# Kernel optimization log

Measured on AMD Instinct MI355X. Metric: run time of the kernel, lower is better.

## Reference

```python
import jax, jax.numpy as jnp
import numpy as np

KERNEL_BANDWIDTH = 0.3
STEP_SIZE = 0.5
NB_ITERATIONS = 4


def setup_inputs() -> dict:
    key = jax.random.key(0)
    # B x D x H x W pixel embeddings
    x_in = jax.random.normal(key, (2, 64, 96, 96), dtype=jnp.float32)
    return {"x_in": x_in}


def reference(x_in):
    B, D, H, W = x_in.shape
    N = H * W
    x0 = x_in.reshape(B, D, N)

    def body(x, _):
        # Gaussian-like kernel K[i,j] = exp(bw * <x_i, x_j>), symmetric NxN per batch
        K = jnp.exp(KERNEL_BANDWIDTH * jnp.einsum('bdn,bdm->bnm', x, x))  # (B,N,N)
        # torch: diag(K^T @ 1) then inverse of that diagonal == 1/column-sums
        colsum = jnp.sum(K, axis=1)  # (B,N)
        # x @ (K diag(1/colsum)): column-normalized weighted mean of embeddings
        xk = jnp.einsum('bdn,bnm->bdm', x, K) / colsum[:, None, :]
        x_new = STEP_SIZE * xk + (1.0 - STEP_SIZE) * x
        return x_new, x_new

    _, ys = jax.lax.scan(body, x0, None, length=NB_ITERATIONS)  # (I,B,D,N)
    allx = jnp.concatenate([x0[None], ys], axis=0)  # (I+1,B,D,N)
    # B x (I+1) x D x H x W
    return jnp.transpose(allx, (1, 0, 2, 3)).reshape(B, NB_ITERATIONS + 1, D, H, W)
```

## Files before the change

kernel.cpp:

```cpp
#include <hip/hip_runtime.h>
#include <hip/hip_bf16.h>

constexpr int B_    = 2;
constexpr int N_    = 9216;
constexpr int ITERS = 4;

constexpr int MTQ     = 128;
constexpr int MBF     = N_ / MTQ;
constexpr int KS      = 4;
constexpr int KEYS_WG = N_ / KS;
constexpr int KT      = 64;
constexpr int KTILES  = KEYS_WG / KT;
constexpr int NWG     = B_ * MBF * KS;
constexpr int PB      = 144;
constexpr int CGRID   = B_ * (N_ / 32);

constexpr float STEP = 0.5f;
constexpr float C2   = 0.43280851226668905f;

using short8   = __attribute__((ext_vector_type(8))) short;
using float16v = __attribute__((ext_vector_type(16))) float;
typedef __attribute__((ext_vector_type(2))) __bf16 bf16x2;

__device__ __forceinline__ unsigned short f2bf(float f) {
  union { float f; unsigned u; } v; v.f = f;
  unsigned u = v.u;
  unsigned r = (u + 0x7fffu + ((u >> 16) & 1u)) >> 16;
  return (unsigned short)r;
}

#if __has_builtin(__builtin_amdgcn_cvt_pk_bf16_f32)
__device__ __forceinline__ unsigned pk2bf(float a, float b) {
  bf16x2 r = __builtin_amdgcn_cvt_pk_bf16_f32(a, b);
  union { bf16x2 h; unsigned u; } v; v.h = r; return v.u;
}
#else
__device__ __forceinline__ unsigned pk2bf(float a, float b) {
  return (unsigned)f2bf(a) | ((unsigned)f2bf(b) << 16);
}
#endif

__device__ __forceinline__ float csum2(unsigned u, float cs) {
#if __has_builtin(__builtin_amdgcn_fdot2_f32_bf16)
  union { unsigned x; bf16x2 h; } a, o;
  a.x = u; o.x = 0x3f803f80u;
  return __builtin_amdgcn_fdot2_f32_bf16(a.h, o.h, cs, false);
#else
  union { unsigned u; float f; } lo, hi;
  lo.u = u << 16; hi.u = u & 0xffff0000u;
  return cs + lo.f + hi.f;
#endif
}

__device__ __forceinline__ void dma16(const unsigned short* g,
                                      unsigned short* lds_base, int lane) {
#if __has_builtin(__builtin_amdgcn_global_load_lds)
  __builtin_amdgcn_global_load_lds(
      (const __attribute__((address_space(1))) unsigned int*)g,
      (__attribute__((address_space(3))) unsigned int*)lds_base, 16, 0, 0);
#else
  *(int4*)((char*)lds_base + lane * 16) = *(const int4*)g;
#endif
}

__global__ void prep_kernel(const float* __restrict__ xin, float* __restrict__ out,
                            unsigned short* __restrict__ XT,
                            unsigned short* __restrict__ Xbf)
{
  const int bx = blockIdx.x;
  const int nb = bx % PB, b = bx / PB;
  const int n0 = nb * 64;
  const int tid = threadIdx.x;
  __shared__ float tile[64 * 65];

  #pragma unroll
  for (int r = 0; r < 16; ++r) {
    int idx = r * 256 + tid;
    int d = idx >> 6, j = idx & 63;
    float v = xin[((size_t)b * 64 + d) * N_ + n0 + j];
    out[(((size_t)b * 5 + 0) * 64 + d) * N_ + n0 + j] = v;
    Xbf[((size_t)b * 64 + d) * N_ + n0 + j] = f2bf(v);
    tile[d * 65 + j] = v;
  }
  __syncthreads();
  #pragma unroll
  for (int r = 0; r < 16; ++r) {
    int idx = r * 256 + tid;
    int nl = idx >> 6, d = idx & 63;
    XT[((size_t)b * N_ + n0 + nl) * 64 + d] = f2bf(tile[d * 65 + nl]);
  }
}

__global__ void __launch_bounds__(256, 3) flash_kernel(
    const unsigned short* __restrict__ XT,
    const unsigned short* __restrict__ Xbf,
    float* __restrict__ pacc, float* __restrict__ pcs)
{
  const int bx   = blockIdx.x;
  const int ks   = bx & 3;
  const int mb   = (bx >> 2) % MBF;
  const int b    = bx / (MBF * KS);
  const int tid  = threadIdx.x;
  const int wave = tid >> 6, lane = tid & 63;
  const int c = lane & 31, h = lane >> 5;
  const int cp = (c & 0x13) | ((c & 4) << 1) | ((c & 8) >> 1);
  const int m0 = mb * MTQ;
  const int bpaddr = (lane ^ 32) << 2;

  const unsigned short* XTb = XT  + (size_t)b * N_ * 64;
  const unsigned short* Xb  = Xbf + (size_t)b * 64 * N_;

  __shared__ __align__(16) unsigned short sXT[2][KT * 64];
  __shared__ __align__(16) unsigned short sXB[2][64 * KT];

  const int rr = lane >> 3, sc = lane & 7;
  const int gc = sc ^ rr;

  const int n0g0 = ks * KEYS_WG;

  const unsigned short* xtp  = XTb + (size_t)(n0g0 + wave * 16 + rr) * 64 + gc * 8;
  const unsigned short* xbp0 = Xb  + (size_t)(wave * 16 + rr) * N_ + n0g0 + gc * 8;
  const unsigned short* xbp1 = xbp0 + (size_t)8 * N_;

  auto stage = [&](int buf, const unsigned short* xt_,
                   const unsigned short* xb0_, const unsigned short* xb1_) {
    unsigned short* lt = &sXT[buf][wave * 16 * 64];
    unsigned short* lb = &sXB[buf][wave * 16 * 64];
    dma16(xt_,       lt,       lane);
    dma16(xt_ + 512, lt + 512, lane);
    dma16(xb0_,      lb,       lane);
    dma16(xb1_,      lb + 512, lane);
  };

  stage(0, xtp, xbp0, xbp1);
  xtp += KT * 64; xbp0 += KT; xbp1 += KT;

  short8 qf[4];
  #pragma unroll
  for (int k = 0; k < 4; ++k) {
    short8 raw = *(const short8*)(XTb +
        (size_t)(m0 + wave * 32 + c) * 64 + k * 16 + h * 8);
    unsigned o[4];
    const unsigned* rw = (const unsigned*)&raw;
    #pragma unroll
    for (int p4 = 0; p4 < 4; ++p4) {
      union { unsigned u; float f; } lo, hi;
      lo.u = rw[p4] << 16; hi.u = rw[p4] & 0xffff0000u;
      o[p4] = pk2bf(lo.f * C2, hi.f * C2);
    }
    qf[k] = *(const short8*)o;
  }

  const int e = cp & 7;
  const unsigned short* afb[4];
  #pragma unroll
  for (int k = 0; k < 4; ++k)
    afb[k] = &sXT[0][cp * 64 + ((2 * k + h) ^ e) * 8];
  const int ec = c & 7;
  const unsigned short* bfb0[2], * bfb1[2];
  #pragma unroll
  for (int s = 0; s < 2; ++s) {
    bfb0[s] = &sXB[0][c * 64 + ((4 * s +     h) ^ ec) * 8];
    bfb1[s] = &sXB[0][c * 64 + ((4 * s + 2 + h) ^ ec) * 8];
  }

  float16v zv;
  #pragma unroll
  for (int p = 0; p < 16; ++p) zv[p] = 0.f;
  float16v acc[2];
  acc[0] = zv; acc[1] = zv;
  float cs = 0.f;

  __syncthreads();

  #pragma unroll 2
  for (int t = 0; t < KTILES; ++t) {
    const int buf = t & 1;
    if (t + 1 < KTILES) {
      stage(buf ^ 1, xtp, xbp0, xbp1);
      xtp += KT * 64; xbp0 += KT; xbp1 += KT;
    }

    #pragma unroll
    for (int s = 0; s < 2; ++s) {
      short8 af[4];
      #pragma unroll
      for (int k = 0; k < 4; ++k)
        af[k] = *(const short8*)(afb[k] + buf * 4096 + s * 2048);

      float16v S = zv;
      #pragma unroll
      for (int k = 0; k < 4; ++k)
        S = __builtin_amdgcn_mfma_f32_32x32x16_bf16(af[k], qf[k], S, 0, 0, 0);

      unsigned q[8];
      #pragma unroll
      for (int g = 0; g < 8; ++g) {
        float w0 = __builtin_amdgcn_exp2f(S[2 * g]);
        float w1 = __builtin_amdgcn_exp2f(S[2 * g + 1]);
        unsigned u = pk2bf(w0, w1);
        q[g] = u;
        cs = csum2(u, cs);
      }

      union { unsigned d[4]; short8 s8; } a20, a21;
      a20.d[0] = q[0]; a20.d[1] = q[1]; a20.d[2] = q[2]; a20.d[3] = q[3];
      a21.d[0] = q[4]; a21.d[1] = q[5]; a21.d[2] = q[6]; a21.d[3] = q[7];

      short8 b20[2], b21[2];
      #pragma unroll
      for (int dt = 0; dt < 2; ++dt) {
        b20[dt] = *(const short8*)(bfb0[s] + buf * 4096 + dt * 2048);
        b21[dt] = *(const short8*)(bfb1[s] + buf * 4096 + dt * 2048);
      }
      #pragma unroll
      for (int dt = 0; dt < 2; ++dt)
        acc[dt] = __builtin_amdgcn_mfma_f32_32x32x16_bf16(a20.s8, b20[dt], acc[dt], 0, 0, 0);
      #pragma unroll
      for (int dt = 0; dt < 2; ++dt)
        acc[dt] = __builtin_amdgcn_mfma_f32_32x32x16_bf16(a21.s8, b21[dt], acc[dt], 0, 0, 0);
    }

    __syncthreads();
  }

  union { float f; int i; } cu; cu.f = cs;
  cu.i = __builtin_amdgcn_ds_bpermute(bpaddr, cu.i);
  float cst = cs + cu.f;
  if (h == 0) pcs[(size_t)bx * 128 + wave * 32 + c] = cst;

  float* pw = pacc + (size_t)bx * (MTQ * 64);
  #pragma unroll
  for (int dt = 0; dt < 2; ++dt)
    #pragma unroll
    for (int p = 0; p < 16; ++p) {
      int m = wave * 32 + (p & 3) + 8 * (p >> 2) + 4 * h;
      pw[m * 64 + dt * 32 + c] = acc[dt][p];
    }
}

__global__ void combine_kernel(const float* __restrict__ pacc,
                               const float* __restrict__ pcs,
                               float* __restrict__ out,
                               unsigned short* __restrict__ XT,
                               unsigned short* __restrict__ Xbf, int t)
{
  const int bx  = blockIdx.x;
  const int q32 = bx % 288, b = bx / 288;
  const int m0  = q32 * 32;
  const int base = (b * MBF + (q32 >> 2)) * KS;
  const int poff = (q32 & 3) * 2048;
  const int coff = (q32 & 3) * 32;
  const int tid = threadIdx.x;
  __shared__ float accs[32 * 65];
  __shared__ float cstl[32];

  #pragma unroll
  for (int r = 0; r < 2; ++r) {
    int i4 = r * 256 + tid;
    float4 s = make_float4(0.f, 0.f, 0.f, 0.f);
    #pragma unroll
    for (int k = 0; k < KS; ++k) {
      const float4* p = (const float4*)(pacc + (size_t)(base + k) * 8192 + poff);
      float4 v = p[i4];
      s.x += v.x; s.y += v.y; s.z += v.z; s.w += v.w;
    }
    int m = i4 >> 4, d0 = (i4 & 15) * 4;
    accs[m * 65 + d0 + 0] = s.x;
    accs[m * 65 + d0 + 1] = s.y;
    accs[m * 65 + d0 + 2] = s.z;
    accs[m * 65 + d0 + 3] = s.w;
  }
  if (tid < 32) {
    float cv = 0.f;
    #pragma unroll
    for (int k = 0; k < KS; ++k) cv += pcs[(size_t)(base + k) * 128 + coff + tid];
    cstl[tid] = cv;
  }
  __syncthreads();

  #pragma unroll
  for (int r = 0; r < 4; ++r) {
    int idx = r * 256 + tid;
    int ml = (idx & 15) * 2, d = idx >> 4;
    float a0 = accs[ml * 65 + d], a1 = accs[(ml + 1) * 65 + d];
    size_t obase = (((size_t)b * 5 + t) * 64 + d) * N_ + m0 + ml;
    float2 xc = *(const float2*)(out + obase);
    float v0 = STEP * (a0 / cstl[ml])     + (1.f - STEP) * xc.x;
    float v1 = STEP * (a1 / cstl[ml + 1]) + (1.f - STEP) * xc.y;
    *(float2*)(out + obase + (size_t)64 * N_) = make_float2(v0, v1);
    *(unsigned*)(Xbf + ((size_t)b * 64 + d) * N_ + m0 + ml) = pk2bf(v0, v1);
    accs[ml * 65 + d] = v0; accs[(ml + 1) * 65 + d] = v1;
  }
  __syncthreads();

  #pragma unroll
  for (int r = 0; r < 4; ++r) {
    int idx = r * 256 + tid;
    int m = idx >> 5, d = (idx & 31) * 2;
    *(unsigned*)(XT + ((size_t)b * N_ + m0 + m) * 64 + d)
        = pk2bf(accs[m * 65 + d], accs[m * 65 + d + 1]);
  }
}

extern "C" void kernel_launch(void* const* d_in, const int* in_sizes, int n_in,
                              void* d_out, int out_size, void* d_ws, size_t ws_size,
                              hipStream_t stream)
{
  (void)in_sizes; (void)n_in; (void)out_size; (void)ws_size;
  const float* xin = (const float*)d_in[0];
  float* out = (float*)d_out;
  char* ws = (char*)d_ws;

  unsigned short* XT  = (unsigned short*)(ws);
  unsigned short* Xbf = (unsigned short*)(ws +  2359296);
  float*          pacc = (float*)(ws +  4718592);
  float*          pcs  = (float*)(ws + 23592960);

  prep_kernel<<<B_ * PB, 256, 0, stream>>>(xin, out, XT, Xbf);
  for (int t = 0; t < ITERS; ++t) {
    flash_kernel<<<NWG, 256, 0, stream>>>(XT, Xbf, pacc, pcs);
    combine_kernel<<<CGRID, 256, 0, stream>>>(pacc, pcs, out, XT, Xbf, t);
  }
}
```

Measured before the change: 373.8 us.

## Software-pipeline PV MFMAs one tile behind QK/exp to overlap stages

Restructures the key-tile loop so the P·V MFMAs for tile t-1 run alongside the QK MFMA and exp work for tile t. The packed exp weights and B fragments are carried across iterations in registers, with a prologue and epilogue around the loop. The column-sum accumulator is split in two to shorten the dependency chain. The goal is to hide exp/VALU latency behind matrix work, at the cost of more live registers and possibly lower occupancy.

New measurement: 368.8 us. About the same (-1.3%).

```diff
diff --git a/kernel.cpp b/kernel.cpp
--- a/kernel.cpp
+++ b/kernel.cpp
@@ -169,60 +169,77 @@
   for (int p = 0; p < 16; ++p) zv[p] = 0.f;
   float16v acc[2];
   acc[0] = zv; acc[1] = zv;
-  float cs = 0.f;
-
-  __syncthreads();
-
-  #pragma unroll 2
-  for (int t = 0; t < KTILES; ++t) {
-    const int buf = t & 1;
-    if (t + 1 < KTILES) {
-      stage(buf ^ 1, xtp, xbp0, xbp1);
-      xtp += KT * 64; xbp0 += KT; xbp1 += KT;
-    }
-
+  float cs0 = 0.f, cs1 = 0.f;
+
+  unsigned qwp[2][8];
+  short8 b20c[2][2], b21c[2][2];
+
+  auto QKEXP = [&](int buf) {
     #pragma unroll
     for (int s = 0; s < 2; ++s) {
       short8 af[4];
       #pragma unroll
       for (int k = 0; k < 4; ++k)
         af[k] = *(const short8*)(afb[k] + buf * 4096 + s * 2048);
-
       float16v S = zv;
       #pragma unroll
       for (int k = 0; k < 4; ++k)
         S = __builtin_amdgcn_mfma_f32_32x32x16_bf16(af[k], qf[k], S, 0, 0, 0);
-
-      unsigned q[8];
       #pragma unroll
       for (int g = 0; g < 8; ++g) {
         float w0 = __builtin_amdgcn_exp2f(S[2 * g]);
         float w1 = __builtin_amdgcn_exp2f(S[2 * g + 1]);
         unsigned u = pk2bf(w0, w1);
-        q[g] = u;
-        cs = csum2(u, cs);
+        qwp[s][g] = u;
+        if (s) cs1 = csum2(u, cs1); else cs0 = csum2(u, cs0);
       }
-
+    }
+  };
+  auto BREAD = [&](int buf) {
+    #pragma unroll
+    for (int s = 0; s < 2; ++s) {
+      b20c[s][0] = *(const short8*)(bfb0[s] + buf * 4096);
+      b20c[s][1] = *(const short8*)(bfb0[s] + buf * 4096 + 2048);
+      b21c[s][0] = *(const short8*)(bfb1[s] + buf * 4096);
+      b21c[s][1] = *(const short8*)(bfb1[s] + buf * 4096 + 2048);
+    }
+  };
+  auto PV = [&]() {
+    #pragma unroll
+    for (int s = 0; s < 2; ++s) {
       union { unsigned d[4]; short8 s8; } a20, a21;
-      a20.d[0] = q[0]; a20.d[1] = q[1]; a20.d[2] = q[2]; a20.d[3] = q[3];
-      a21.d[0] = q[4]; a21.d[1] = q[5]; a21.d[2] = q[6]; a21.d[3] = q[7];
-
-      short8 b20[2], b21[2];
       #pragma unroll
-      for (int dt = 0; dt < 2; ++dt) {
-        b20[dt] = *(const short8*)(bfb0[s] + buf * 4096 + dt * 2048);
-        b21[dt] = *(const short8*)(bfb1[s] + buf * 4096 + dt * 2048);
-      }
-      #pragma unroll
-      for (int dt = 0; dt < 2; ++dt)
-        acc[dt] = __builtin_amdgcn_mfma_f32_32x32x16_bf16(a20.s8, b20[dt], acc[dt], 0, 0, 0);
-      #pragma unroll
-      for (int dt = 0; dt < 2; ++dt)
-        acc[dt] = __builtin_amdgcn_mfma_f32_32x32x16_bf16(a21.s8, b21[dt], acc[dt], 0, 0, 0);
-    }
-
+      for (int j = 0; j < 4; ++j) { a20.d[j] = qwp[s][j]; a21.d[j] = qwp[s][4 + j]; }
+      acc[0] = __builtin_amdgcn_mfma_f32_32x32x16_bf16(a20.s8, b20c[s][0], acc[0], 0, 0, 0);
+      acc[1] = __builtin_amdgcn_mfma_f32_32x32x16_bf16(a20.s8, b20c[s][1], acc[1], 0, 0, 0);
+      acc[0] = __builtin_amdgcn_mfma_f32_32x32x16_bf16(a21.s8, b21c[s][0], acc[0], 0, 0, 0);
+      acc[1] = __builtin_amdgcn_mfma_f32_32x32x16_bf16(a21.s8, b21c[s][1], acc[1], 0, 0, 0);
+    }
+  };
+
+  __syncthreads();
+
+  stage(1, xtp, xbp0, xbp1);
+  xtp += KT * 64; xbp0 += KT; xbp1 += KT;
+  QKEXP(0);
+  BREAD(0);
+  __syncthreads();
+
+  #pragma unroll 2
+  for (int t = 1; t < KTILES; ++t) {
+    const int buf = t & 1;
+    if (t + 1 < KTILES) {
+      stage(buf ^ 1, xtp, xbp0, xbp1);
+      xtp += KT * 64; xbp0 += KT; xbp1 += KT;
+    }
+    PV();
+    QKEXP(buf);
+    BREAD(buf);
     __syncthreads();
   }
+
+  PV();
+  float cs = cs0 + cs1;
 
   union { float f; int i; } cu; cu.f = cs;
   cu.i = __builtin_amdgcn_ds_bpermute(bpaddr, cu.i);
```
